# Optimization experiments

Measured on AMD Instinct MI355X. Metric: run time of the kernel, lower is better.

The kernel has to match this reference:

```python
import jax, jax.numpy as jnp
import numpy as np

IN_FEAT = 66; D_MODEL = 512; KS = 10; DCT_N = 20; NUM_STAGE = 2; BN_EPS = 1e-5
HID = D_MODEL; GCN_IN = 2 * DCT_N


def get_dct_matrix(N):
    k = np.arange(N)[:, None]; i = np.arange(N)[None, :]
    w = np.full((N, 1), np.sqrt(2.0 / N)); w[0, 0] = np.sqrt(1.0 / N)
    dct = (w * np.cos(np.pi * (i + 0.5) * k / N)).astype(np.float32)
    idct = np.linalg.inv(dct).astype(np.float32)
    return jnp.asarray(dct), jnp.asarray(idct)


def conv1d(x, w):
    # x: [B, Cin, L], w: [Cout, Cin, K] -> [B, Cout, L-K+1]
    return jax.lax.conv_general_dilated(x, w, (1,), 'VALID', dimension_numbers=('NCH', 'OIH', 'NCH'))


def _forward(src, Wq1, Wq2, Wk1, Wk2, gc1_W, gc1_att, gc1_b, bn1_g, bn1_b,
             gcb_W, gcb_att, gcb_b, gcb_bn_g, gcb_bn_b, gc7_W, gc7_att, gc7_b,
             output_n, input_n):
    bs = src.shape[0]
    src = src[:, :input_n]                                  # [B, 50, F]
    vl = KS + output_n                                      # 35
    vn = input_n - KS - output_n + 1                        # 16
    dct_m, idct_m = get_dct_matrix(vl)

    key_in = jnp.swapaxes(src, 1, 2)[:, :, :input_n - output_n] / 1000.0   # [B, F, 25]
    query_in = jnp.swapaxes(src, 1, 2)[:, :, -KS:] / 1000.0                # [B, F, 10]

    # overlapping sliding windows -> per-window DCT coefficients
    idx = np.arange(vl)[None, :] + np.arange(vn)[:, None]   # [vn, vl]
    val = src[:, idx]                                       # [B, vn, vl, F]
    val = jnp.einsum('kv,bnvf->bnfk', dct_m[:DCT_N], val).reshape(bs, vn, IN_FEAT * DCT_N)

    key = jax.nn.relu(conv1d(jax.nn.relu(conv1d(key_in, Wk1)), Wk2))       # [B, D, vn]
    query = jax.nn.relu(conv1d(jax.nn.relu(conv1d(query_in, Wq1)), Wq2))   # [B, D, 1]

    score = jnp.einsum('bdq,bdn->bqn', query, key) + 1e-15                 # [B, 1, vn]
    att = score / jnp.sum(score, axis=2, keepdims=True)                    # sum-normalized attention
    dct_att = jnp.einsum('bqn,bnf->bqf', att, val)[:, 0].reshape(bs, IN_FEAT, DCT_N)

    # last KS frames + last frame repeated output_n times
    idx2 = np.concatenate([np.arange(input_n - KS, input_n), np.full(output_n, input_n - 1)])
    input_gcn = src[:, idx2]                                               # [B, vl, F]
    dct_in = jnp.swapaxes(jnp.einsum('kv,bvf->bkf', dct_m[:DCT_N], input_gcn), 1, 2)  # [B, F, DCT_N]
    x = jnp.concatenate([dct_in, dct_att], axis=-1)                        # [B, F, 2*DCT_N]

    # ---- GCN (eval mode: dropout off, BN with fresh running stats mean=0, var=1) ----
    def gc(y, W, A, bias):
        return jnp.einsum('nm,bmf->bnf', A, y @ W) + bias

    def bn(y, g, be):
        b_, n_, f_ = y.shape
        v = y.reshape(b_, n_ * f_)
        v = v * (g / np.float32(np.sqrt(1.0 + BN_EPS))) + be
        return v.reshape(b_, n_, f_)

    y = jnp.tanh(bn(gc(x, gc1_W, gc1_att, gc1_b), bn1_g, bn1_b))
    for st in range(NUM_STAGE):
        y0 = y
        y = jnp.tanh(bn(gc(y, gcb_W[st, 0], gcb_att[st, 0], gcb_b[st, 0]), gcb_bn_g[st, 0], gcb_bn_b[st, 0]))
        y = jnp.tanh(bn(gc(y, gcb_W[st, 1], gcb_att[st, 1], gcb_b[st, 1]), gcb_bn_g[st, 1], gcb_bn_b[st, 1]))
        y = y + y0
    dct_out = gc(y, gc7_W, gc7_att, gc7_b) + x                             # [B, F, 2*DCT_N]

    out = jnp.einsum('vk,bfk->bvf', idct_m[:, :DCT_N], dct_out[:, :, :DCT_N])  # [B, vl, F]
    return out[:, :, None, :]                                              # [B, vl, itera=1, F]


def setup_inputs():
    key = jax.random.key(0)
    ks = jax.random.split(key, 11)
    bs = 512; s = 0.05; f32 = jnp.float32
    return {
        'src': jax.random.normal(ks[0], (bs, 50, IN_FEAT), f32),
        'Wq1': jax.random.normal(ks[1], (D_MODEL, IN_FEAT, 6), f32) * s,
        'Wq2': jax.random.normal(ks[2], (D_MODEL, D_MODEL, 5), f32) * s,
        'Wk1': jax.random.normal(ks[3], (D_MODEL, IN_FEAT, 6), f32) * s,
        'Wk2': jax.random.normal(ks[4], (D_MODEL, D_MODEL, 5), f32) * s,
        'gc1_W': jax.random.normal(ks[5], (GCN_IN, HID), f32) * s,
        'gc1_att': jax.random.normal(ks[6], (IN_FEAT, IN_FEAT), f32) * s,
        'gc1_b': jnp.zeros((HID,), f32),
        'bn1_g': jnp.ones((IN_FEAT * HID,), f32),
        'bn1_b': jnp.zeros((IN_FEAT * HID,), f32),
        'gcb_W': jax.random.normal(ks[7], (NUM_STAGE, 2, HID, HID), f32) * s,
        'gcb_att': jax.random.normal(ks[8], (NUM_STAGE, 2, IN_FEAT, IN_FEAT), f32) * s,
        'gcb_b': jnp.zeros((NUM_STAGE, 2, HID), f32),
        'gcb_bn_g': jnp.ones((NUM_STAGE, 2, IN_FEAT * HID), f32),
        'gcb_bn_b': jnp.zeros((NUM_STAGE, 2, IN_FEAT * HID), f32),
        'gc7_W': jax.random.normal(ks[9], (HID, GCN_IN), f32) * s,
        'gc7_att': jax.random.normal(ks[10], (IN_FEAT, IN_FEAT), f32) * s,
        'gc7_b': jnp.zeros((GCN_IN,), f32),
        'output_n': 25,
        'input_n': 50,
    }


def reference(src, Wq1, Wq2, Wk1, Wk2, gc1_W, gc1_att, gc1_b, bn1_g, bn1_b,
              gcb_W, gcb_att, gcb_b, gcb_bn_g, gcb_bn_b, gc7_W, gc7_att, gc7_b,
              output_n, input_n):
    return _forward(src, Wq1, Wq2, Wk1, Wk2, gc1_W, gc1_att, gc1_b, bn1_g, bn1_b,
                    gcb_W, gcb_att, gcb_b, gcb_bn_g, gcb_bn_b, gc7_W, gc7_att, gc7_b,
                    output_n, input_n)
```

## Files before the change

kernel.cpp:

```cpp
#include <hip/hip_runtime.h>
#include <math.h>

#define PI_D 3.14159265358979323846

#define BSZ   512
#define NODE  66
#define VL    35
#define DCTN  20

static constexpr float BN_INVS = 0.99999500003749969f;

typedef unsigned short u16;
using bf16x8 = __attribute__((ext_vector_type(8))) short;
using f32x4  = __attribute__((ext_vector_type(4))) float;

__device__ inline u16 f2bf(float f) {
    union { float f; unsigned int u; } v; v.f = f;
    unsigned int r = v.u + 0x7FFFu + ((v.u >> 16) & 1u);
    return (u16)(r >> 16);
}
__device__ inline float bf2f(u16 b) {
    union { unsigned int u; float f; } v; v.u = ((unsigned int)b) << 16;
    return v.f;
}

__global__ void dct_kernel(float* __restrict__ dct20) {
    int i = blockIdx.x * blockDim.x + threadIdx.x;
    if (i < DCTN * VL) {
        int k = i / VL, v = i - k * VL;
        double w = (k == 0) ? sqrt(1.0 / VL) : sqrt(2.0 / VL);
        dct20[i] = (float)(w * cos(PI_D * (v + 0.5) * k / (double)VL));
    }
}

__global__ void cvt_gcb(const float* __restrict__ W, u16* __restrict__ Wt) {
    int l = blockIdx.y;
    int i = blockIdx.x * 256 + threadIdx.x;
    int n = i >> 9, k = i & 511;
    Wt[(size_t)l * 262144 + i] = f2bf(W[(size_t)l * 262144 + (size_t)k * 512 + n]);
}
__global__ void cvt_gc1(const float* __restrict__ W, u16* __restrict__ Wt) {
    int i = blockIdx.x * 256 + threadIdx.x;
    int n = i >> 6, k = i & 63;
    Wt[i] = (k < 40) ? f2bf(W[k * 512 + n]) : (u16)0;
}
__global__ void cvt_gc7(const float* __restrict__ W, u16* __restrict__ Wt) {
    int i = blockIdx.x * 256 + threadIdx.x;
    int n = i >> 9, k = i & 511;
    Wt[i] = (n < 20) ? f2bf(W[k * 40 + n]) : (u16)0;
}
__global__ void cvt_w1(const float* __restrict__ W, u16* __restrict__ Wt) {
    int i = blockIdx.x * 256 + threadIdx.x;
    int d = i / 416, k = i - d * 416;
    float v = 0.f;
    if (k < 396) { int h = k / 66, c = k - h * 66; v = W[d * 396 + c * 6 + h]; }
    Wt[i] = f2bf(v);
}
__global__ void cvt_w2(const float* __restrict__ W, u16* __restrict__ Wt) {
    int i = blockIdx.x * 256 + threadIdx.x;
    int d = i / 2560, k = i - d * 2560;
    int h = k >> 9, c = k & 511;
    Wt[i] = f2bf(W[(size_t)d * 2560 + c * 5 + h]);
}
__global__ void cvt_att(const float* __restrict__ gc1A, const float* __restrict__ gcbA,
                        const float* __restrict__ gc7A, u16* __restrict__ Abf) {
    int l = blockIdx.y;
    int i = blockIdx.x * 256 + threadIdx.x;
    if (i < 8320) {
        int r = i / 104, c = i - (i / 104) * 104;
        float v = 0.f;
        if (r < 66 && c < 66) {
            const float* A = (l == 0) ? gc1A : (l <= 4 ? gcbA + (size_t)(l - 1) * 4356 : gc7A);
            v = A[r * 66 + c];
        }
        Abf[(size_t)l * 8320 + i] = f2bf(v);
    }
}

template<int EPI>
__global__ __launch_bounds__(256) void gc_fused(const u16* __restrict__ Y,
                                                const u16* __restrict__ Wt,
                                                const u16* __restrict__ Ab,
                                                void* __restrict__ Yout, int K,
                                                const float* __restrict__ bias,
                                                const float* __restrict__ g,
                                                const float* __restrict__ be,
                                                const u16* __restrict__ yres,
                                                const float* __restrict__ xres) {
    __shared__ u16 As[144][40];
    __shared__ u16 Bs[128][40];
    __shared__ u16 zT[128][168];
    const int tid = threadIdx.x;
    const int b0 = blockIdx.x * 2;
    const int n0 = blockIdx.y * 128;
    const int lane = tid & 63, w = tid >> 6;
    const int row16 = lane & 15, grp = lane >> 4;

    for (int i = tid; i < 128 * 36; i += 256) {
        int f = i / 36, j = i - (i / 36) * 36;
        int c = (j < 6) ? (66 + j) : (132 + j);
        zT[f][c] = 0;
    }

    const int sr = tid >> 1, sq = (tid & 1) * 16;
    long r1 = (long)b0 * 66 + sr;        if (r1 > 33791) r1 = 33791;
    long r2 = (long)b0 * 66 + 128 + sr;  if (r2 > 33791) r2 = 33791;
    const u16* ap1 = Y + (size_t)r1 * K + sq;
    const u16* ap2 = Y + (size_t)r2 * K + sq;
    const u16* bp  = Wt + (size_t)(n0 + sr) * K + sq;

    f32x4 acc[9][2] = {};
    for (int k0 = 0; k0 < K; k0 += 32) {
        *(bf16x8*)&As[sr][sq]     = *(const bf16x8*)(ap1 + k0);
        *(bf16x8*)&As[sr][sq + 8] = *(const bf16x8*)(ap1 + k0 + 8);
        if (tid < 32) {
            *(bf16x8*)&As[128 + sr][sq]     = *(const bf16x8*)(ap2 + k0);
            *(bf16x8*)&As[128 + sr][sq + 8] = *(const bf16x8*)(ap2 + k0 + 8);
        }
        *(bf16x8*)&Bs[sr][sq]     = *(const bf16x8*)(bp + k0);
        *(bf16x8*)&Bs[sr][sq + 8] = *(const bf16x8*)(bp + k0 + 8);
        __syncthreads();
        bf16x8 a[9], b[2];
#pragma unroll
        for (int mt = 0; mt < 9; ++mt) a[mt] = *(const bf16x8*)&As[mt * 16 + row16][grp * 8];
#pragma unroll
        for (int nt = 0; nt < 2; ++nt) b[nt] = *(const bf16x8*)&Bs[w * 32 + nt * 16 + row16][grp * 8];
#pragma unroll
        for (int mt = 0; mt < 9; ++mt)
#pragma unroll
            for (int nt = 0; nt < 2; ++nt)
                acc[mt][nt] = __builtin_amdgcn_mfma_f32_16x16x32_bf16(a[mt], b[nt], acc[mt][nt], 0, 0, 0);
        __syncthreads();
    }

#pragma unroll
    for (int mt = 0; mt < 9; ++mt) {
        int m = mt * 16 + grp * 4;
        if (m < 132) {
#pragma unroll
            for (int nt = 0; nt < 2; ++nt) {
                int f = w * 32 + nt * 16 + row16;
                u16 e0 = f2bf(acc[mt][nt][0]), e1 = f2bf(acc[mt][nt][1]);
                u16 e2 = f2bf(acc[mt][nt][2]), e3 = f2bf(acc[mt][nt][3]);
                if (m + 3 < 66 || m >= 66) {
                    int col = (m < 66) ? m : m + 6;
                    *(unsigned int*)&zT[f][col]     = (unsigned int)e0 | ((unsigned int)e1 << 16);
                    *(unsigned int*)&zT[f][col + 2] = (unsigned int)e2 | ((unsigned int)e3 << 16);
                } else {
                    zT[f][64] = e0; zT[f][65] = e1; zT[f][72] = e2; zT[f][73] = e3;
                }
            }
        }
    }

    bf16x8 aA[5][3];
#pragma unroll
    for (int mt = 0; mt < 5; ++mt)
#pragma unroll
        for (int k2 = 0; k2 < 3; ++k2)
            aA[mt][k2] = *(const bf16x8*)&Ab[(mt * 16 + row16) * 104 + k2 * 32 + grp * 8];
    __syncthreads();

    f32x4 acc2[2][5][2] = {};
#pragma unroll
    for (int bb = 0; bb < 2; ++bb) {
        const int base = bb * 72;
#pragma unroll
        for (int k2 = 0; k2 < 3; ++k2) {
            bf16x8 bz[2];
#pragma unroll
            for (int ft = 0; ft < 2; ++ft)
                bz[ft] = *(const bf16x8*)&zT[w * 32 + ft * 16 + row16][base + k2 * 32 + grp * 8];
#pragma unroll
            for (int mt = 0; mt < 5; ++mt)
#pragma unroll
                for (int ft = 0; ft < 2; ++ft)
                    acc2[bb][mt][ft] = __builtin_amdgcn_mfma_f32_16x16x32_bf16(aA[mt][k2], bz[ft], acc2[bb][mt][ft], 0, 0, 0);
        }
    }

#pragma unroll
    for (int bb = 0; bb < 2; ++bb) {
        const int bidx = b0 + bb;
#pragma unroll
        for (int mt = 0; mt < 5; ++mt) {
            int nb = mt * 16 + grp * 4;
#pragma unroll
            for (int ft = 0; ft < 2; ++ft) {
                int c = n0 + w * 32 + ft * 16 + row16;
#pragma unroll
                for (int j = 0; j < 4; ++j) {
                    int n = nb + j;
                    if (n < 66) {
                        float v = acc2[bb][mt][ft][j];
                        if constexpr (EPI == 4) {
                            if (c < 20)
                                ((float*)Yout)[(size_t)bidx * 1320 + n * 20 + c] =
                                    v + bias[c] + xres[(size_t)bidx * 2640 + n * 40 + c];
                        } else {
                            int gi = n * 512 + c;
                            float z = v + bias[c];
                            float t = tanhf(z * (g[gi] * BN_INVS) + be[gi]);
                            if constexpr (EPI == 3) t += bf2f(yres[((size_t)bidx * 66 + n) * 512 + c]);
                            ((u16*)Yout)[((size_t)bidx * 66 + n) * 512 + c] = f2bf(t);
                        }
                    }
                }
            }
        }
    }
}

template<int ASRC, int EPI, int TOUT, int TIN, int T0>
__global__ __launch_bounds__(256) void gemm_uni(const void* __restrict__ Asrc,
                                                const u16* __restrict__ Bt,
                                                void* __restrict__ Cout,
                                                int M, int K, int Nvalid, int ldc) {
    __shared__ u16 As[128][40];
    __shared__ u16 Bs[128][40];
    const int tid = threadIdx.x;
    const int r0 = blockIdx.x * 128, n0 = blockIdx.y * 128;
    const int lane = tid & 63, w = tid >> 6;
    const int wr = (w >> 1) * 64, wc = (w & 1) * 64;
    const int row16 = lane & 15, grp = lane >> 4;
    const int sr = tid >> 1, sq = (tid & 1) * 16;

    const u16* ap = nullptr;
    const float* apf = nullptr;
    if constexpr (ASRC == 1) {
        int R = r0 + sr; int b = R / TOUT, t = R - b * TOUT;
        ap = (const u16*)Asrc + ((size_t)b * TIN + t) * 512 + sq;
    } else {
        int R = r0 + sr; int b = R / TOUT, t = R - b * TOUT;
        apf = (const float*)Asrc + (size_t)b * 3300 + (T0 + t) * 66 + sq;
    }
    const u16* bp = Bt + (size_t)(n0 + sr) * K + sq;

    f32x4 acc[4][4] = {};
    for (int k0 = 0; k0 < K; k0 += 32) {
        if constexpr (ASRC == 1) {
            *(bf16x8*)&As[sr][sq]     = *(const bf16x8*)(ap + k0);
            *(bf16x8*)&As[sr][sq + 8] = *(const bf16x8*)(ap + k0 + 8);
        } else {
#pragma unroll
            for (int j = 0; j < 16; ++j) {
                int k = k0 + sq + j;
                float vin = 0.f;
                if (k < 396) vin = apf[k0 + j];
                As[sr][sq + j] = f2bf(vin * 1e-3f);
            }
        }
        *(bf16x8*)&Bs[sr][sq]     = *(const bf16x8*)(bp + k0);
        *(bf16x8*)&Bs[sr][sq + 8] = *(const bf16x8*)(bp + k0 + 8);
        __syncthreads();
        bf16x8 a[4], b[4];
#pragma unroll
        for (int m = 0; m < 4; ++m) a[m] = *(const bf16x8*)&As[wr + m * 16 + row16][grp * 8];
#pragma unroll
        for (int n = 0; n < 4; ++n) b[n] = *(const bf16x8*)&Bs[wc + n * 16 + row16][grp * 8];
#pragma unroll
        for (int m = 0; m < 4; ++m)
#pragma unroll
            for (int n = 0; n < 4; ++n)
                acc[m][n] = __builtin_amdgcn_mfma_f32_16x16x32_bf16(a[m], b[n], acc[m][n], 0, 0, 0);
        __syncthreads();
    }
#pragma unroll
    for (int m = 0; m < 4; ++m) {
        int rb = r0 + wr + m * 16 + grp * 4;
#pragma unroll
        for (int n = 0; n < 4; ++n) {
            int c = n0 + wc + n * 16 + row16;
            if (c < Nvalid) {
#pragma unroll
                for (int j = 0; j < 4; ++j) {
                    float v = fmaxf(acc[m][n][j], 0.f);
                    if constexpr (EPI == 0) ((u16*)Cout)[(size_t)(rb + j) * ldc + c] = f2bf(v);
                    else                    ((float*)Cout)[(size_t)(rb + j) * ldc + c] = v;
                }
            }
        }
    }
}

__global__ __launch_bounds__(256) void att_kernel(const float* __restrict__ qT,
                                                  const float* __restrict__ kT,
                                                  float* __restrict__ att) {
    const int b = blockIdx.x, tid = threadIdx.x;
    __shared__ float part[256];
    __shared__ float sc[16];
    int n = tid >> 4, j = tid & 15;
    const float* q = qT + b * 512;
    const float* k = kT + b * 8192 + n * 512;
    float acc = 0.f;
    for (int d = j; d < 512; d += 16) acc += q[d] * k[d];
    part[tid] = acc;
    __syncthreads();
    if (tid < 16) {
        float s = 0.f;
        for (int jj = 0; jj < 16; ++jj) s += part[tid * 16 + jj];
        sc[tid] = s + 1e-15f;
    }
    __syncthreads();
    if (tid == 0) {
        float tot = 0.f;
        for (int nn = 0; nn < 16; ++nn) tot += sc[nn];
        float inv = 1.f / tot;
        for (int nn = 0; nn < 16; ++nn) att[b * 16 + nn] = sc[nn] * inv;
    }
}

__global__ __launch_bounds__(256) void xbuild(const float* __restrict__ src,
                                              const float* __restrict__ att,
                                              const float* __restrict__ dct20,
                                              float* __restrict__ x,
                                              u16* __restrict__ xbf) {
    const int b = blockIdx.x, tid = threadIdx.x;
    __shared__ float s_src[50 * 66];
    __shared__ float s_sacc[VL * 66];
    __shared__ float s_d[DCTN * VL];
    __shared__ float s_att[16];
    for (int i = tid; i < 3300; i += 256) s_src[i] = src[b * 3300 + i];
    for (int i = tid; i < DCTN * VL; i += 256) s_d[i] = dct20[i];
    if (tid < 16) s_att[tid] = att[b * 16 + tid];
    __syncthreads();
    for (int i = tid; i < VL * 66; i += 256) {
        int v = i / 66, f = i - (i / 66) * 66;
        float a = 0.f;
#pragma unroll
        for (int n = 0; n < 16; ++n) a += s_att[n] * s_src[(n + v) * 66 + f];
        s_sacc[i] = a;
    }
    __syncthreads();
    for (int i = tid; i < 66 * DCTN; i += 256) {
        int f = i / DCTN, kq = i - (i / DCTN) * DCTN;
        float din = 0.f, datt = 0.f;
        for (int v = 0; v < VL; ++v) {
            float dv = s_d[kq * VL + v];
            int t2 = (v < 10) ? (40 + v) : 49;
            din += dv * s_src[t2 * 66 + f];
            datt += dv * s_sacc[v * 66 + f];
        }
        x[b * 2640 + f * 40 + kq] = din;
        x[b * 2640 + f * 40 + 20 + kq] = datt;
        xbf[(size_t)b * 4224 + f * 64 + kq] = f2bf(din);
        xbf[(size_t)b * 4224 + f * 64 + 20 + kq] = f2bf(datt);
    }
    for (int i = tid; i < 66 * 24; i += 256) {
        int f = i / 24, kp = 40 + (i - (i / 24) * 24);
        xbf[(size_t)b * 4224 + f * 64 + kp] = 0;
    }
}

__global__ __launch_bounds__(256) void final_out(const float* __restrict__ dctout,
                                                 const float* __restrict__ dct20,
                                                 float* __restrict__ out) {
    const int b = blockIdx.x, tid = threadIdx.x;
    __shared__ float ds[DCTN * VL];
    __shared__ float dos[66 * 20];
    for (int i = tid; i < DCTN * VL; i += 256) ds[i] = dct20[i];
    for (int i = tid; i < 1320; i += 256) dos[i] = dctout[(size_t)b * 1320 + i];
    __syncthreads();
    for (int o = tid; o < VL * 66; o += 256) {
        int v = o / 66, f = o - (o / 66) * 66;
        float acc = 0.f;
#pragma unroll
        for (int k = 0; k < DCTN; ++k) acc += ds[k * VL + v] * dos[f * 20 + k];
        out[(size_t)b * 2310 + o] = acc;
    }
}

extern "C" void kernel_launch(void* const* d_in, const int* in_sizes, int n_in,
                              void* d_out, int out_size, void* d_ws, size_t ws_size,
                              hipStream_t stream) {
    const float* src     = (const float*)d_in[0];
    const float* Wq1     = (const float*)d_in[1];
    const float* Wq2     = (const float*)d_in[2];
    const float* Wk1     = (const float*)d_in[3];
    const float* Wk2     = (const float*)d_in[4];
    const float* gc1_W   = (const float*)d_in[5];
    const float* gc1_att = (const float*)d_in[6];
    const float* gc1_b   = (const float*)d_in[7];
    const float* bn1_g   = (const float*)d_in[8];
    const float* bn1_b   = (const float*)d_in[9];
    const float* gcb_W   = (const float*)d_in[10];
    const float* gcb_att = (const float*)d_in[11];
    const float* gcb_b   = (const float*)d_in[12];
    const float* gcb_g   = (const float*)d_in[13];
    const float* gcb_be  = (const float*)d_in[14];
    const float* gc7_W   = (const float*)d_in[15];
    const float* gc7_att = (const float*)d_in[16];
    const float* gc7_b   = (const float*)d_in[17];
    float* out = (float*)d_out;

    unsigned char* base = (unsigned char*)d_ws;
    size_t off = 0;
    auto take = [&](size_t bytes) -> void* {
        void* p = base + off;
        off += (bytes + 255) & ~(size_t)255;
        return p;
    };
    u16*   yA     = (u16*)take((size_t)33792 * 512 * 2);
    u16*   yB     = (u16*)take((size_t)33792 * 512 * 2);
    float* xb     = (float*)take((size_t)512 * 2640 * 4);
    u16*   xbf    = (u16*)take((size_t)512 * 4224 * 2);
    float* dct20  = (float*)take(2800);
    float* dctout = (float*)take((size_t)512 * 1320 * 4);
    u16*   key1   = (u16*)take((size_t)512 * 20 * 512 * 2);
    u16*   q1     = (u16*)take((size_t)512 * 5 * 512 * 2);
    float* keyT   = (float*)take((size_t)8192 * 512 * 4);
    float* queryT = (float*)take((size_t)512 * 512 * 4);
    float* attw   = (float*)take((size_t)512 * 16 * 4);
    u16*   WtGcb  = (u16*)take((size_t)4 * 512 * 512 * 2);
    u16*   WtGc1  = (u16*)take((size_t)512 * 64 * 2);
    u16*   WtGc7  = (u16*)take((size_t)128 * 512 * 2);
    u16*   WtW1k  = (u16*)take((size_t)512 * 416 * 2);
    u16*   WtW1q  = (u16*)take((size_t)512 * 416 * 2);
    u16*   WtW2k  = (u16*)take((size_t)512 * 2560 * 2);
    u16*   WtW2q  = (u16*)take((size_t)512 * 2560 * 2);
    u16*   Abf    = (u16*)take((size_t)6 * 8320 * 2);

    dct_kernel<<<2, 384, 0, stream>>>(dct20);
    cvt_att<<<dim3(33, 6), 256, 0, stream>>>(gc1_att, gcb_att, gc7_att, Abf);
    cvt_gcb<<<dim3(1024, 4), 256, 0, stream>>>(gcb_W, WtGcb);
    cvt_gc1<<<128, 256, 0, stream>>>(gc1_W, WtGc1);
    cvt_gc7<<<256, 256, 0, stream>>>(gc7_W, WtGc7);
    cvt_w1<<<832, 256, 0, stream>>>(Wk1, WtW1k);
    cvt_w1<<<832, 256, 0, stream>>>(Wq1, WtW1q);
    cvt_w2<<<5120, 256, 0, stream>>>(Wk2, WtW2k);
    cvt_w2<<<5120, 256, 0, stream>>>(Wq2, WtW2q);

    gemm_uni<2, 0, 20, 25, 0><<<dim3(80, 4), 256, 0, stream>>>(
        src, WtW1k, key1, 10240, 416, 512, 512);
    gemm_uni<2, 0, 5, 10, 40><<<dim3(20, 4), 256, 0, stream>>>(
        src, WtW1q, q1, 2560, 416, 512, 512);
    gemm_uni<1, 1, 16, 20, 0><<<dim3(64, 4), 256, 0, stream>>>(
        key1, WtW2k, keyT, 8192, 2560, 512, 512);
    gemm_uni<1, 1, 1, 5, 0><<<dim3(4, 4), 256, 0, stream>>>(
        q1, WtW2q, queryT, 512, 2560, 512, 512);
    att_kernel<<<BSZ, 256, 0, stream>>>(queryT, keyT, attw);
    xbuild<<<BSZ, 256, 0, stream>>>(src, attw, dct20, xb, xbf);

    gc_fused<2><<<dim3(256, 4), 256, 0, stream>>>(
        xbf, WtGc1, Abf, yA, 64, gc1_b, bn1_g, bn1_b, nullptr, nullptr);

    for (int st = 0; st < 2; ++st) {
        const u16* W0 = WtGcb + (size_t)(st * 2 + 0) * 262144;
        const u16* W1 = WtGcb + (size_t)(st * 2 + 1) * 262144;
        const u16* A0 = Abf + (size_t)(1 + st * 2) * 8320;
        const u16* A1 = Abf + (size_t)(2 + st * 2) * 8320;
        const float* b0  = gcb_b + (size_t)(st * 2 + 0) * 512;
        const float* b1  = gcb_b + (size_t)(st * 2 + 1) * 512;
        const float* g0  = gcb_g + (size_t)(st * 2 + 0) * 33792;
        const float* g1  = gcb_g + (size_t)(st * 2 + 1) * 33792;
        const float* be0 = gcb_be + (size_t)(st * 2 + 0) * 33792;
        const float* be1 = gcb_be + (size_t)(st * 2 + 1) * 33792;
        gc_fused<2><<<dim3(256, 4), 256, 0, stream>>>(
            yA, W0, A0, yB, 512, b0, g0, be0, nullptr, nullptr);
        gc_fused<3><<<dim3(256, 4), 256, 0, stream>>>(
            yB, W1, A1, yA, 512, b1, g1, be1, yA, nullptr);
    }

    gc_fused<4><<<dim3(256, 1), 256, 0, stream>>>(
        yA, WtGc7, Abf + (size_t)5 * 8320, dctout, 512, gc7_b, nullptr, nullptr, nullptr, xb);
    final_out<<<BSZ, 256, 0, stream>>>(dctout, dct20, out);
}
```

Before: 808.4 us.

## Stage GEMM tiles via direct global-to-LDS loads with plane layout and shared smem

```diff
diff --git a/kernel.cpp b/kernel.cpp
--- a/kernel.cpp
+++ b/kernel.cpp
@@ -11,16 +11,24 @@
 static constexpr float BN_INVS = 0.99999500003749969f;
 
 typedef unsigned short u16;
+typedef unsigned int   u32;
 using bf16x8 = __attribute__((ext_vector_type(8))) short;
 using f32x4  = __attribute__((ext_vector_type(4))) float;
 
+#define AS1 __attribute__((address_space(1)))
+#define AS3 __attribute__((address_space(3)))
+
+__device__ __forceinline__ void gl16(const u16* g, u16* l) {
+    __builtin_amdgcn_global_load_lds((const AS1 u32*)g, (AS3 u32*)l, 16, 0, 0);
+}
+
 __device__ inline u16 f2bf(float f) {
-    union { float f; unsigned int u; } v; v.f = f;
-    unsigned int r = v.u + 0x7FFFu + ((v.u >> 16) & 1u);
+    union { float f; u32 u; } v; v.f = f;
+    u32 r = v.u + 0x7FFFu + ((v.u >> 16) & 1u);
     return (u16)(r >> 16);
 }
 __device__ inline float bf2f(u16 b) {
-    union { unsigned int u; float f; } v; v.u = ((unsigned int)b) << 16;
+    union { u32 u; float f; } v; v.u = ((u32)b) << 16;
     return v.f;
 }
 
@@ -78,60 +86,69 @@
 }
 
 template<int EPI>
-__global__ __launch_bounds__(256) void gc_fused(const u16* __restrict__ Y,
-                                                const u16* __restrict__ Wt,
-                                                const u16* __restrict__ Ab,
-                                                void* __restrict__ Yout, int K,
-                                                const float* __restrict__ bias,
-                                                const float* __restrict__ g,
-                                                const float* __restrict__ be,
-                                                const u16* __restrict__ yres,
-                                                const float* __restrict__ xres) {
-    __shared__ u16 As[144][40];
-    __shared__ u16 Bs[128][40];
-    __shared__ u16 zT[128][168];
+__global__ __launch_bounds__(256, 4) void gc_fused(const u16* __restrict__ Y,
+                                                   const u16* __restrict__ Wt,
+                                                   const u16* __restrict__ Ab,
+                                                   void* __restrict__ Yout, int K,
+                                                   const float* __restrict__ bias,
+                                                   const float* __restrict__ g,
+                                                   const float* __restrict__ be,
+                                                   const u16* __restrict__ yres,
+                                                   const float* __restrict__ xres) {
+    __shared__ u16 smem[19624];
+    u16* AsF = smem;
+    u16* BsF = smem + 4608;
+    u16* zT  = smem;
+
     const int tid = threadIdx.x;
     const int b0 = blockIdx.x * 2;
     const int n0 = blockIdx.y * 128;
     const int lane = tid & 63, w = tid >> 6;
     const int row16 = lane & 15, grp = lane >> 4;
 
-    for (int i = tid; i < 128 * 36; i += 256) {
-        int f = i / 36, j = i - (i / 36) * 36;
+    int k0;
+    auto stageA = [&](int c) {
+        int flat = c * 1024 + lane * 16;
+        int plane = flat / 2304;
+        int row = (flat - plane * 2304) >> 4;
+        long grow = (long)b0 * 66 + row; if (grow > 33791) grow = 33791;
+        gl16(Y + (size_t)grow * K + k0 + plane * 8, AsF + c * 512);
+    };
+    auto stageB = [&](int c) {
+        int row = ((c & 1) << 6) + lane;
+        gl16(Wt + (size_t)(n0 + row) * K + k0 + (c >> 1) * 8, BsF + c * 512);
+    };
+
+    f32x4 acc[9][2] = {};
+    for (k0 = 0; k0 < K; k0 += 32) {
+        stageA(w); stageA(w + 4); if (w == 0) stageA(8);
+        stageB(2 * w); stageB(2 * w + 1);
+        __syncthreads();
+        const int aoff = grp * 1152 + row16 * 8;
+        const int boff = grp * 1024 + (w * 32 + row16) * 8;
+        bf16x8 b[2];
+#pragma unroll
+        for (int nt = 0; nt < 2; ++nt) b[nt] = *(const bf16x8*)&BsF[boff + nt * 128];
+#pragma unroll
+        for (int mc = 0; mc < 3; ++mc) {
+            bf16x8 a[3];
+#pragma unroll
+            for (int i = 0; i < 3; ++i) a[i] = *(const bf16x8*)&AsF[aoff + (mc * 3 + i) * 128];
+#pragma unroll
+            for (int i = 0; i < 3; ++i)
+#pragma unroll
+                for (int nt = 0; nt < 2; ++nt)
+                    acc[mc * 3 + i][nt] = __builtin_amdgcn_mfma_f32_16x16x32_bf16(a[i], b[nt], acc[mc * 3 + i][nt], 0, 0, 0);
+        }
+        __syncthreads();
+    }
+
+    for (int i = tid; i < 128 * 20; i += 256) {
+        int f = i / 20, j = i - (i / 20) * 20;
         int c = (j < 6) ? (66 + j) : (132 + j);
-        zT[f][c] = 0;
-    }
-
-    const int sr = tid >> 1, sq = (tid & 1) * 16;
-    long r1 = (long)b0 * 66 + sr;        if (r1 > 33791) r1 = 33791;
-    long r2 = (long)b0 * 66 + 128 + sr;  if (r2 > 33791) r2 = 33791;
-    const u16* ap1 = Y + (size_t)r1 * K + sq;
-    const u16* ap2 = Y + (size_t)r2 * K + sq;
-    const u16* bp  = Wt + (size_t)(n0 + sr) * K + sq;
-
-    f32x4 acc[9][2] = {};
-    for (int k0 = 0; k0 < K; k0 += 32) {
-        *(bf16x8*)&As[sr][sq]     = *(const bf16x8*)(ap1 + k0);
-        *(bf16x8*)&As[sr][sq + 8] = *(const bf16x8*)(ap1 + k0 + 8);
-        if (tid < 32) {
-            *(bf16x8*)&As[128 + sr][sq]     = *(const bf16x8*)(ap2 + k0);
-            *(bf16x8*)&As[128 + sr][sq + 8] = *(const bf16x8*)(ap2 + k0 + 8);
-        }
-        *(bf16x8*)&Bs[sr][sq]     = *(const bf16x8*)(bp + k0);
-        *(bf16x8*)&Bs[sr][sq + 8] = *(const bf16x8*)(bp + k0 + 8);
-        __syncthreads();
-        bf16x8 a[9], b[2];
-#pragma unroll
-        for (int mt = 0; mt < 9; ++mt) a[mt] = *(const bf16x8*)&As[mt * 16 + row16][grp * 8];
-#pragma unroll
-        for (int nt = 0; nt < 2; ++nt) b[nt] = *(const bf16x8*)&Bs[w * 32 + nt * 16 + row16][grp * 8];
-#pragma unroll
-        for (int mt = 0; mt < 9; ++mt)
-#pragma unroll
-            for (int nt = 0; nt < 2; ++nt)
-                acc[mt][nt] = __builtin_amdgcn_mfma_f32_16x16x32_bf16(a[mt], b[nt], acc[mt][nt], 0, 0, 0);
-        __syncthreads();
-    }
+        zT[f * 152 + c] = 0;
+    }
+    for (int i = tid; i < 168; i += 256) zT[19456 + i] = 0;
 
 #pragma unroll
     for (int mt = 0; mt < 9; ++mt) {
@@ -144,10 +161,11 @@
                 u16 e2 = f2bf(acc[mt][nt][2]), e3 = f2bf(acc[mt][nt][3]);
                 if (m + 3 < 66 || m >= 66) {
                     int col = (m < 66) ? m : m + 6;
-                    *(unsigned int*)&zT[f][col]     = (unsigned int)e0 | ((unsigned int)e1 << 16);
-                    *(unsigned int*)&zT[f][col + 2] = (unsigned int)e2 | ((unsigned int)e3 << 16);
+                    *(u32*)&zT[f * 152 + col]     = (u32)e0 | ((u32)e1 << 16);
+                    *(u32*)&zT[f * 152 + col + 2] = (u32)e2 | ((u32)e3 << 16);
                 } else {
-                    zT[f][64] = e0; zT[f][65] = e1; zT[f][72] = e2; zT[f][73] = e3;
+                    zT[f * 152 + 64] = e0; zT[f * 152 + 65] = e1;
+                    zT[f * 152 + 72] = e2; zT[f * 152 + 73] = e3;
                 }
             }
         }
@@ -170,7 +188,7 @@
             bf16x8 bz[2];
 #pragma unroll
             for (int ft = 0; ft < 2; ++ft)
-                bz[ft] = *(const bf16x8*)&zT[w * 32 + ft * 16 + row16][base + k2 * 32 + grp * 8];
+                bz[ft] = *(const bf16x8*)&zT[(w * 32 + ft * 16 + row16) * 152 + base + k2 * 32 + grp * 8];
 #pragma unroll
             for (int mt = 0; mt < 5; ++mt)
 #pragma unroll
@@ -216,8 +234,8 @@
                                                 const u16* __restrict__ Bt,
                                                 void* __restrict__ Cout,
                                                 int M, int K, int Nvalid, int ldc) {
-    __shared__ u16 As[128][40];
-    __shared__ u16 Bs[128][40];
+    __shared__ u16 AsF[4096];
+    __shared__ u16 BsF[4096];
     const int tid = threadIdx.x;
     const int r0 = blockIdx.x * 128, n0 = blockIdx.y * 128;
     const int lane = tid & 63, w = tid >> 6;
@@ -225,39 +243,45 @@
     const int row16 = lane & 15, grp = lane >> 4;
     const int sr = tid >> 1, sq = (tid & 1) * 16;
 
-    const u16* ap = nullptr;
     const float* apf = nullptr;
-    if constexpr (ASRC == 1) {
-        int R = r0 + sr; int b = R / TOUT, t = R - b * TOUT;
-        ap = (const u16*)Asrc + ((size_t)b * TIN + t) * 512 + sq;
-    } else {
+    if constexpr (ASRC == 2) {
         int R = r0 + sr; int b = R / TOUT, t = R - b * TOUT;
         apf = (const float*)Asrc + (size_t)b * 3300 + (T0 + t) * 66 + sq;
     }
-    const u16* bp = Bt + (size_t)(n0 + sr) * K + sq;
 
     f32x4 acc[4][4] = {};
     for (int k0 = 0; k0 < K; k0 += 32) {
         if constexpr (ASRC == 1) {
-            *(bf16x8*)&As[sr][sq]     = *(const bf16x8*)(ap + k0);
-            *(bf16x8*)&As[sr][sq + 8] = *(const bf16x8*)(ap + k0 + 8);
+#pragma unroll
+            for (int i = 0; i < 2; ++i) {
+                int c = 2 * w + i;
+                int row = ((c & 1) << 6) + lane;
+                int R = r0 + row; int b = R / TOUT, t = R - b * TOUT;
+                gl16((const u16*)Asrc + ((size_t)b * TIN + t) * 512 + k0 + (c >> 1) * 8,
+                     AsF + c * 512);
+            }
         } else {
 #pragma unroll
             for (int j = 0; j < 16; ++j) {
                 int k = k0 + sq + j;
                 float vin = 0.f;
                 if (k < 396) vin = apf[k0 + j];
-                As[sr][sq + j] = f2bf(vin * 1e-3f);
+                int col = sq + j;
+                AsF[(col >> 3) * 1024 + sr * 8 + (col & 7)] = f2bf(vin * 1e-3f);
             }
         }
-        *(bf16x8*)&Bs[sr][sq]     = *(const bf16x8*)(bp + k0);
-        *(bf16x8*)&Bs[sr][sq + 8] = *(const bf16x8*)(bp + k0 + 8);
+#pragma unroll
+        for (int i = 0; i < 2; ++i) {
+            int c = 2 * w + i;
+            int row = ((c & 1) << 6) + lane;
+            gl16(Bt + (size_t)(n0 + row) * K + k0 + (c >> 1) * 8, BsF + c * 512);
+        }
         __syncthreads();
         bf16x8 a[4], b[4];
 #pragma unroll
-        for (int m = 0; m < 4; ++m) a[m] = *(const bf16x8*)&As[wr + m * 16 + row16][grp * 8];
-#pragma unroll
-        for (int n = 0; n < 4; ++n) b[n] = *(const bf16x8*)&Bs[wc + n * 16 + row16][grp * 8];
+        for (int m = 0; m < 4; ++m) a[m] = *(const bf16x8*)&AsF[grp * 1024 + (wr + m * 16 + row16) * 8];
+#pragma unroll
+        for (int n = 0; n < 4; ++n) b[n] = *(const bf16x8*)&BsF[grp * 1024 + (wc + n * 16 + row16) * 8];
 #pragma unroll
         for (int m = 0; m < 4; ++m)
 #pragma unroll
```

Measured after the change: 939.4 us. 16.2% more time.
